# Performance work log

Hardware: AMD Instinct MI355X
Metric: run time of the kernel (lower is better)

The kernel has to match this reference:

```python
import jax, jax.numpy as jnp
import numpy as np

N = 20000      # nodes
E = 320000     # edges (avg degree 16)
IN = 512       # input feature dim
HID = 64       # hidden_dim
NH = 8         # n_heads
NC = 20        # n_classes
NG = 64        # graphs in batch
EPS = 1e-5     # batchnorm eps


def setup_inputs() -> dict:
    key = jax.random.key(0)
    ks = jax.random.split(key, 32)
    rn = lambda k, shape, s=0.05: (jax.random.normal(k, shape, jnp.float32) * s)
    inp = {
        "x": rn(ks[0], (N, IN), 1.0),
        "src": jax.random.randint(ks[1], (E,), 0, N),
        "dst": jax.random.randint(ks[2], (E,), 0, N),
        "graph_ids": jnp.sort(jax.random.randint(ks[3], (N,), 0, NG)),
        "n_graphs": NG,
        # encoder
        "W_enc": rn(ks[4], (IN, HID)), "b_enc": jnp.zeros((HID,), jnp.float32),
        # GAT layer 0
        "fc_W0": rn(ks[5], (HID, NH * HID)),
        "attn_l0": rn(ks[6], (NH, HID)), "attn_r0": rn(ks[7], (NH, HID)),
        "res_W0": rn(ks[8], (HID, NH * HID)),
        "bias0": jnp.zeros((NH * HID,), jnp.float32),
        "dp_W0": rn(ks[9], (NH * HID, HID)), "dp_b0": jnp.zeros((HID,), jnp.float32),
        # GAT layer 1
        "fc_W1": rn(ks[10], (HID, NH * HID)),
        "attn_l1": rn(ks[11], (NH, HID)), "attn_r1": rn(ks[12], (NH, HID)),
        "res_W1": rn(ks[13], (HID, NH * HID)),
        "bias1": jnp.zeros((NH * HID,), jnp.float32),
        "dp_W1": rn(ks[14], (NH * HID, HID)), "dp_b1": jnp.zeros((HID,), jnp.float32),
        # batchnorm affine
        "gamma": jnp.ones((2 * HID,), jnp.float32), "beta": jnp.zeros((2 * HID,), jnp.float32),
        # global attention pooling gate
        "gate_W": rn(ks[15], (2 * HID, 1)), "gate_b": jnp.zeros((1,), jnp.float32),
        # classifier
        "cls_W": rn(ks[16], (2 * HID, NC)), "cls_b": jnp.zeros((NC,), jnp.float32),
    }
    return inp


def gat_conv(h, fc_W, attn_l, attn_r, res_W, bias, src, dst, n_nodes):
    # DGL GATConv: fc -> per-head scalar scores -> edge softmax over incoming
    # edges -> weighted sum -> residual + bias -> leaky_relu activation.
    nh, d = attn_l.shape
    feat = (h @ fc_W).reshape(n_nodes, nh, d)              # [N,H,D]
    el = jnp.sum(feat * attn_l[None], axis=-1)             # [N,H]
    er = jnp.sum(feat * attn_r[None], axis=-1)             # [N,H]
    e = jax.nn.leaky_relu(el[src] + er[dst], 0.2)          # [E,H]
    m = jax.ops.segment_max(e, dst, num_segments=n_nodes)  # segment softmax
    ex = jnp.exp(e - m[dst])
    denom = jax.ops.segment_sum(ex, dst, num_segments=n_nodes)
    a = ex / denom[dst]                                    # [E,H]
    msg = feat[src] * a[:, :, None]                        # [E,H,D]  (dominant)
    rst = jax.ops.segment_sum(msg, dst, num_segments=n_nodes)  # [N,H,D]
    rst = rst + (h @ res_W).reshape(n_nodes, nh, d) + bias.reshape(nh, d)
    return jax.nn.leaky_relu(rst, 0.01)  # F.leaky_relu default slope


def reference(x, W_enc, b_enc,
              fc_W0, attn_l0, attn_r0, res_W0, bias0, dp_W0, dp_b0,
              fc_W1, attn_l1, attn_r1, res_W1, bias1, dp_W1, dp_b1,
              gamma, beta, gate_W, gate_b, cls_W, cls_b,
              src, dst, graph_ids, n_graphs):
    n_nodes = x.shape[0]
    he = x @ W_enc + b_enc                                  # encoder [N,HID]
    h = he
    h = gat_conv(h, fc_W0, attn_l0, attn_r0, res_W0, bias0, src, dst, n_nodes)
    h = h.reshape(n_nodes, -1) @ dp_W0 + dp_b0              # down_proj 0
    h = gat_conv(h, fc_W1, attn_l1, attn_r1, res_W1, bias1, src, dst, n_nodes)
    h = h.reshape(n_nodes, -1) @ dp_W1 + dp_b1              # down_proj 1
    hg = jnp.concatenate([h, he], axis=1)                   # [N,2*HID]
    # BatchNorm1d (training-mode batch stats, biased variance)
    mu = jnp.mean(hg, axis=0)
    var = jnp.var(hg, axis=0)
    hg = (hg - mu) * jax.lax.rsqrt(var + EPS) * gamma + beta
    # GlobalAttentionPooling: per-graph softmax over node gates
    gate = hg @ gate_W + gate_b                             # [N,1]
    gm = jax.ops.segment_max(gate, graph_ids, num_segments=n_graphs)
    ge = jnp.exp(gate - gm[graph_ids])
    gden = jax.ops.segment_sum(ge, graph_ids, num_segments=n_graphs)
    alpha = ge / gden[graph_ids]                            # [N,1]
    readout = jax.ops.segment_sum(alpha * hg, graph_ids, num_segments=n_graphs)
    return readout @ cls_W + cls_b                          # [NG,NC]
```

## Files before the change

### kernel.cpp

```cpp
#include <hip/hip_runtime.h>
#include <hip/hip_bf16.h>

#define MROWS   20000
#define N_EDGES 320000
#define DIN     512
#define HID     64
#define NH      8
#define ND      512
#define NCLS    20
#define NG      64
#define BN_EPS  1e-5f
#define PCH     16
#define BNB     256

typedef __hip_bfloat16 bf16;
typedef __attribute__((ext_vector_type(8))) short s16x8;
typedef __attribute__((ext_vector_type(4))) float f32x4;

enum { TF32 = 0, TBF16 = 1, TMODE = 2 };

__device__ __forceinline__ int getmode(const void* gamma) {
    return *(const unsigned*)gamma != 0x3F800000u;
}

__device__ __forceinline__ float ld_f32(const void* p, size_t i) { return ((const float*)p)[i]; }
__device__ __forceinline__ float ld_b16(const void* p, size_t i) { return __bfloat162float(((const bf16*)p)[i]); }

template<int T>
__device__ __forceinline__ float ldT(const void* p, size_t i, int bf) {
    if constexpr (T == TF32) return ld_f32(p, i);
    else if constexpr (T == TBF16) return ld_b16(p, i);
    else return bf ? ld_b16(p, i) : ld_f32(p, i);
}
template<int T>
__device__ __forceinline__ void stT(void* p, size_t i, int bf, float v) {
    if constexpr (T == TF32) ((float*)p)[i] = v;
    else if constexpr (T == TBF16) ((bf16*)p)[i] = __float2bfloat16(v);
    else { if (bf) ((bf16*)p)[i] = __float2bfloat16(v); else ((float*)p)[i] = v; }
}

__device__ __forceinline__ float bfbits2f(short s) {
    return __uint_as_float(((unsigned)(unsigned short)s) << 16);
}
__device__ __forceinline__ short f2bfbits(float v) {
    bf16 b = __float2bfloat16(v);
    return *reinterpret_cast<short*>(&b);
}

struct TP { const void* src[7]; bf16* dst[7]; int K[7]; };
__global__ void transpose7_kernel(TP tp, const void* __restrict__ gamma) {
    const int bf = getmode(gamma);
    int id = blockIdx.y;
    int i = blockIdx.x * 256 + threadIdx.x;
    int K = tp.K[id];
    int N = (DIN * HID) / K;
    int n = i / K, k = i - n * K;
    tp.dst[id][i] = __float2bfloat16(ldT<TMODE>(tp.src[id], (size_t)k * N + n, bf));
}

__global__ void convx_kernel(const void* __restrict__ x, bf16* __restrict__ xb,
                             const void* __restrict__ gamma) {
    if (getmode(gamma)) return;
    const int total4 = MROWS * DIN / 4;
    for (int i4 = blockIdx.x * 256 + threadIdx.x; i4 < total4; i4 += gridDim.x * 256) {
        float4 v = ((const float4*)x)[i4];
        int i = i4 * 4;
        xb[i + 0] = __float2bfloat16(v.x);
        xb[i + 1] = __float2bfloat16(v.y);
        xb[i + 2] = __float2bfloat16(v.z);
        xb[i + 3] = __float2bfloat16(v.w);
    }
}

__global__ void hist_kernel(const int* __restrict__ keys, int* __restrict__ counts, int n) {
    int i = blockIdx.x * 256 + threadIdx.x;
    if (i < n) atomicAdd(&counts[keys[i]], 1);
}

__global__ void gsearch_kernel(const int* __restrict__ gids, int* __restrict__ goffs) {
    int g = threadIdx.x;
    if (g > NG) return;
    int lo = 0, hi = MROWS;
    while (lo < hi) {
        int mid = (lo + hi) >> 1;
        if (gids[mid] < g) lo = mid + 1; else hi = mid;
    }
    goffs[g] = lo;
}

__global__ __launch_bounds__(1024)
void scan_kernel(const int* __restrict__ in, int* __restrict__ out) {
    const int C = 20;
    int t = threadIdx.x;
    int beg = t * C; if (beg > MROWS) beg = MROWS;
    int end = beg + C; if (end > MROWS) end = MROWS;
    int s = 0;
    for (int i = beg; i < end; ++i) s += in[i];
    int lane = t & 63, wid = t >> 6;
    int ps = s;
    #pragma unroll
    for (int o = 1; o < 64; o <<= 1) { int u = __shfl_up(ps, o, 64); if (lane >= o) ps += u; }
    __shared__ int wsum[16];
    if (lane == 63) wsum[wid] = ps;
    __syncthreads();
    if (wid == 0 && lane < 16) {
        int u = wsum[lane];
        #pragma unroll
        for (int o = 1; o < 16; o <<= 1) { int v = __shfl_up(u, o, 64); if (lane >= o) u += v; }
        wsum[lane] = u;
    }
    __syncthreads();
    int carry = ps - s + (wid > 0 ? wsum[wid - 1] : 0);
    int run = carry;
    for (int i = beg; i < end; ++i) { out[i] = run; run += in[i]; }
    if (t == 0) out[MROWS] = N_EDGES;
}

__global__ void scatter_kernel(const int* __restrict__ src, const int* __restrict__ dst,
                               const int* __restrict__ offs, int* __restrict__ cursor,
                               int* __restrict__ src_sorted) {
    int e = blockIdx.x * 256 + threadIdx.x;
    if (e < N_EDGES) {
        int d = dst[e];
        int pos = offs[d] + atomicAdd(&cursor[d], 1);
        src_sorted[pos] = src[e];
    }
}

template<int K, int NB, int NTOT>
__global__ __launch_bounds__(256)
void gemm_mfma(const void* __restrict__ Araw, const bf16* __restrict__ Aconv,
               const bf16* __restrict__ BT, const void* __restrict__ bias,
               bf16* __restrict__ C, const void* __restrict__ gamma) {
    const int bf = getmode(gamma);
    const bf16* A = bf ? (const bf16*)Araw : Aconv;
    const int wid  = threadIdx.x >> 6;
    const int lane = threadIdx.x & 63;
    const int quad = lane >> 4;
    const int l16  = lane & 15;
    const int rb = blockIdx.x * 128 + wid * 32;
    const int cb = blockIdx.y * NB;
    constexpr int CT = NB / 16;
    constexpr int KC = K / 32;

    f32x4 acc[2][CT] = {};
    int r0 = rb + l16;       if (r0 >= MROWS) r0 = MROWS - 1;
    int r1 = rb + 16 + l16;  if (r1 >= MROWS) r1 = MROWS - 1;
    const bf16* a0p = A + (size_t)r0 * K + quad * 8;
    const bf16* a1p = A + (size_t)r1 * K + quad * 8;
    const bf16* btp = BT + (size_t)(cb + l16) * K + quad * 8;

    for (int kc = 0; kc < KC; ++kc) {
        s16x8 af0 = *(const s16x8*)(a0p + kc * 32);
        s16x8 af1 = *(const s16x8*)(a1p + kc * 32);
        s16x8 bfr[CT];
        #pragma unroll
        for (int ct = 0; ct < CT; ++ct)
            bfr[ct] = *(const s16x8*)(btp + (size_t)ct * 16 * K + kc * 32);
        #pragma unroll
        for (int ct = 0; ct < CT; ++ct) {
            acc[0][ct] = __builtin_amdgcn_mfma_f32_16x16x32_bf16(af0, bfr[ct], acc[0][ct], 0, 0, 0);
            acc[1][ct] = __builtin_amdgcn_mfma_f32_16x16x32_bf16(af1, bfr[ct], acc[1][ct], 0, 0, 0);
        }
    }
    #pragma unroll
    for (int ct = 0; ct < CT; ++ct) {
        int col = cb + ct * 16 + l16;
        float bb = bias ? ldT<TMODE>(bias, col, bf) : 0.f;
        #pragma unroll
        for (int rt = 0; rt < 2; ++rt) {
            #pragma unroll
            for (int rg = 0; rg < 4; ++rg) {
                int row = rb + rt * 16 + quad * 4 + rg;
                if (row < MROWS)
                    C[(size_t)row * NTOT + col] = __float2bfloat16(acc[rt][ct][rg] + bb);
            }
        }
    }
}

__global__ __launch_bounds__(256)
void gemm_fcres(const bf16* __restrict__ A, const bf16* __restrict__ BT_fc,
                const bf16* __restrict__ BT_res, const void* __restrict__ bias,
                const void* __restrict__ attn_l, const void* __restrict__ attn_r,
                bf16* __restrict__ feat, bf16* __restrict__ rst,
                float* __restrict__ el, float* __restrict__ er,
                const void* __restrict__ gamma) {
    const int bf = getmode(gamma);
    const bool isres = blockIdx.y >= 4;
    const int yy = blockIdx.y & 3;
    const bf16* BT = isres ? BT_res : BT_fc;
    bf16* C = isres ? rst : feat;
    const int wid  = threadIdx.x >> 6;
    const int lane = threadIdx.x & 63;
    const int quad = lane >> 4;
    const int l16  = lane & 15;
    const int rb = blockIdx.x * 128 + wid * 32;
    const int cb = yy * 128;
    constexpr int CT = 8;
    constexpr int K  = HID;
    constexpr int KC = K / 32;

    f32x4 acc[2][CT] = {};
    int r0 = rb + l16;       if (r0 >= MROWS) r0 = MROWS - 1;
    int r1 = rb + 16 + l16;  if (r1 >= MROWS) r1 = MROWS - 1;
    const bf16* a0p = A + (size_t)r0 * K + quad * 8;
    const bf16* a1p = A + (size_t)r1 * K + quad * 8;
    const bf16* btp = BT + (size_t)(cb + l16) * K + quad * 8;

    #pragma unroll
    for (int kc = 0; kc < KC; ++kc) {
        s16x8 af0 = *(const s16x8*)(a0p + kc * 32);
        s16x8 af1 = *(const s16x8*)(a1p + kc * 32);
        s16x8 bfr[CT];
        #pragma unroll
        for (int ct = 0; ct < CT; ++ct)
            bfr[ct] = *(const s16x8*)(btp + (size_t)ct * 16 * K + kc * 32);
        #pragma unroll
        for (int ct = 0; ct < CT; ++ct) {
            acc[0][ct] = __builtin_amdgcn_mfma_f32_16x16x32_bf16(af0, bfr[ct], acc[0][ct], 0, 0, 0);
            acc[1][ct] = __builtin_amdgcn_mfma_f32_16x16x32_bf16(af1, bfr[ct], acc[1][ct], 0, 0, 0);
        }
    }
    #pragma unroll
    for (int ct = 0; ct < CT; ++ct) {
        int col = cb + ct * 16 + l16;
        float bb = isres ? ldT<TMODE>(bias, col, bf) : 0.f;
        #pragma unroll
        for (int rt = 0; rt < 2; ++rt) {
            #pragma unroll
            for (int rg = 0; rg < 4; ++rg) {
                int row = rb + rt * 16 + quad * 4 + rg;
                if (row < MROWS)
                    C[(size_t)row * ND + col] = __float2bfloat16(acc[rt][ct][rg] + bb);
            }
        }
    }
    if (!isres) {
        float al[CT], ar[CT];
        #pragma unroll
        for (int ct = 0; ct < CT; ++ct) {
            int col = cb + ct * 16 + l16;
            al[ct] = ldT<TMODE>(attn_l, col, bf);
            ar[ct] = ldT<TMODE>(attn_r, col, bf);
        }
        #pragma unroll
        for (int rt = 0; rt < 2; ++rt) {
            #pragma unroll
            for (int rg = 0; rg < 4; ++rg) {
                float e0 = 0.f, e1 = 0.f, f0 = 0.f, f1 = 0.f;
                #pragma unroll
                for (int ct = 0; ct < 4; ++ct) {
                    e0 += acc[rt][ct][rg] * al[ct];
                    f0 += acc[rt][ct][rg] * ar[ct];
                    e1 += acc[rt][ct + 4][rg] * al[ct + 4];
                    f1 += acc[rt][ct + 4][rg] * ar[ct + 4];
                }
                #pragma unroll
                for (int o = 1; o < 16; o <<= 1) {
                    e0 += __shfl_xor(e0, o, 64);
                    e1 += __shfl_xor(e1, o, 64);
                    f0 += __shfl_xor(f0, o, 64);
                    f1 += __shfl_xor(f1, o, 64);
                }
                int row = rb + rt * 16 + quad * 4 + rg;
                if (row < MROWS) {
                    if (l16 == 0) { el[row * 8 + 2 * yy] = e0;     er[row * 8 + 2 * yy] = f0; }
                    if (l16 == 1) { el[row * 8 + 2 * yy + 1] = e1; er[row * 8 + 2 * yy + 1] = f1; }
                }
            }
        }
    }
}

__global__ __launch_bounds__(256)
void agg_kernel(const bf16* __restrict__ feat, const float* __restrict__ el,
                const float* __restrict__ er, const int* __restrict__ offs,
                const int* __restrict__ srcs, bf16* __restrict__ rst) {
    int gid = blockIdx.x * 256 + threadIdx.x;
    int n = gid >> 6;
    int l = threadIdx.x & 63;
    if (n >= MROWS) return;
    int hh = l >> 3;
    int hw = l & 7;
    int e0 = offs[n], e1 = offs[n + 1];
    float er_w = er[n * 8 + hw];
    float acc[8] = {0.f, 0.f, 0.f, 0.f, 0.f, 0.f, 0.f, 0.f};
    float den = 0.f;
    const bf16* fcol = feat + l * 8;

    for (int base = e0; base < e1; base += 8) {
        int m = e1 - base; if (m > 8) m = 8;
        int sv = (base + hw < e1) ? srcs[base + hw] : 0;
        int sj = __shfl(sv, l >> 3, 64);
        float sc = el[sj * 8 + hw] + er_w;
        sc = sc > 0.f ? sc : 0.2f * sc;
        float w = ((l >> 3) < m) ? __expf(fminf(sc, 30.f)) : 0.f;
        if (m == 8) {
            s16x8 rows[8];
            float ws[8];
            #pragma unroll
            for (int j = 0; j < 8; ++j) {
                int s = __shfl(sv, j, 64);
                rows[j] = *(const s16x8*)(fcol + (size_t)s * ND);
                ws[j] = __shfl(w, (j << 3) | hh, 64);
            }
            #pragma unroll
            for (int j = 0; j < 8; ++j) {
                den += ws[j];
                #pragma unroll
                for (int k = 0; k < 8; ++k)
                    acc[k] += bfbits2f(rows[j][k]) * ws[j];
            }
        } else {
            for (int j = 0; j < m; ++j) {
                int s = __shfl(sv, j, 64);
                float wj = __shfl(w, (j << 3) | hh, 64);
                s16x8 f8 = *(const s16x8*)(fcol + (size_t)s * ND);
                den += wj;
                #pragma unroll
                for (int k = 0; k < 8; ++k)
                    acc[k] += bfbits2f(f8[k]) * wj;
            }
        }
    }
    float inv = (den > 0.f) ? 1.f / den : 0.f;
    s16x8* rp = (s16x8*)(rst + (size_t)n * ND + l * 8);
    s16x8 rr = *rp;
    s16x8 ro;
    #pragma unroll
    for (int j = 0; j < 8; ++j) {
        float r = bfbits2f(rr[j]) + acc[j] * inv;
        r = r > 0.f ? r : 0.01f * r;
        ro[j] = f2bfbits(r);
    }
    *rp = ro;
}

__global__ void bn_part_kernel(const bf16* __restrict__ h2, const bf16* __restrict__ he,
                               float* __restrict__ psum, float* __restrict__ psq) {
    int t = threadIdx.x;
    int b = blockIdx.x;
    int beg = (int)((long)MROWS * b / BNB);
    int end = (int)((long)MROWS * (b + 1) / BNB);
    const bf16* srcb = (t < 64) ? h2 : he;
    int col = t & 63;
    float s = 0.f, s2 = 0.f;
    for (int r = beg; r < end; ++r) {
        float v = __bfloat162float(srcb[(size_t)r * 64 + col]);
        s += v;
        s2 += v * v;
    }
    psum[b * 128 + t] = s;
    psq[b * 128 + t] = s2;
}

__global__ void bn_reduce_kernel(const float* __restrict__ psum, const float* __restrict__ psq,
                                 const void* __restrict__ gamma, const void* __restrict__ beta,
                                 float* __restrict__ scale, float* __restrict__ shift) {
    const int bf = getmode(gamma);
    int t = threadIdx.x;
    float s = 0.f, s2 = 0.f;
    for (int b = 0; b < BNB; ++b) { s += psum[b * 128 + t]; s2 += psq[b * 128 + t]; }
    float mu = s * (1.f / MROWS);
    float var = s2 * (1.f / MROWS) - mu * mu;
    float inv = rsqrtf(fmaxf(var, 0.f) + BN_EPS);
    float a = ldT<TMODE>(gamma, t, bf) * inv;
    scale[t] = a;
    shift[t] = ldT<TMODE>(beta, t, bf) - mu * a;
}

__global__ __launch_bounds__(256)
void gate_kernel(const bf16* __restrict__ h2, const bf16* __restrict__ he,
                 const float* __restrict__ scale, const float* __restrict__ shift,
                 const void* __restrict__ gate_W, const void* __restrict__ gate_b,
                 float* __restrict__ ge, const void* __restrict__ gamma) {
    const int bf = getmode(gamma);
    int gid = blockIdx.x * 256 + threadIdx.x;
    int r = gid >> 6;
    int l = threadIdx.x & 63;
    if (r >= MROWS) return;
    float v0 = __bfloat162float(h2[(size_t)r * 64 + l]) * scale[l] + shift[l];
    float v1 = __bfloat162float(he[(size_t)r * 64 + l]) * scale[64 + l] + shift[64 + l];
    float s = v0 * ldT<TMODE>(gate_W, l, bf) + v1 * ldT<TMODE>(gate_W, 64 + l, bf);
    #pragma unroll
    for (int o = 32; o > 0; o >>= 1) s += __shfl_xor(s, o, 64);
    if (l == 0) {
        float g = s + ldT<TMODE>(gate_b, 0, bf);
        ge[r] = __expf(fminf(fmaxf(g, -60.f), 30.f));
    }
}

__global__ void pool1_kernel(const bf16* __restrict__ h2, const bf16* __restrict__ he,
                             const float* __restrict__ scale, const float* __restrict__ shift,
                             const float* __restrict__ ge, const int* __restrict__ goffs,
                             float* __restrict__ pacc, float* __restrict__ pden) {
    int g = blockIdx.x;
    int c = blockIdx.y;
    int t = threadIdx.x;
    int r0 = goffs[g], r1 = goffs[g + 1];
    int len = r1 - r0;
    int beg = r0 + (int)((long)len * c / PCH);
    int end = r0 + (int)((long)len * (c + 1) / PCH);
    const bf16* srcb = (t < 64) ? h2 : he;
    int col = t & 63;
    float sc = scale[t], sh = shift[t];
    float acc = 0.f, den = 0.f;
    for (int r = beg; r < end; ++r) {
        float wg = ge[r];
        float v = __bfloat162float(srcb[(size_t)r * 64 + col]) * sc + sh;
        den += wg;
        acc += wg * v;
    }
    pacc[((size_t)g * PCH + c) * 128 + t] = acc;
    if (t == 0) pden[g * PCH + c] = den;
}

__global__ void pool2cls_kernel(const float* __restrict__ pacc, const float* __restrict__ pden,
                                const void* __restrict__ W, const void* __restrict__ b,
                                void* __restrict__ out, const void* __restrict__ gamma) {
    const int bf = getmode(gamma);
    int g = blockIdx.x;
    int t = threadIdx.x;
    float acc = 0.f, den = 0.f;
    #pragma unroll
    for (int c = 0; c < PCH; ++c) {
        acc += pacc[((size_t)g * PCH + c) * 128 + t];
        den += pden[g * PCH + c];
    }
    __shared__ float ro[128];
    ro[t] = (den > 0.f) ? acc / den : 0.f;
    __syncthreads();
    if (t < NCLS) {
        float s = ldT<TMODE>(b, t, bf);
        #pragma unroll 8
        for (int k = 0; k < 128; ++k)
            s += ro[k] * ldT<TMODE>(W, k * NCLS + t, bf);
        stT<TMODE>(out, g * NCLS + t, bf, s);
    }
}

extern "C" void kernel_launch(void* const* d_in, const int* in_sizes, int n_in,
                              void* d_out, int out_size, void* d_ws, size_t ws_size,
                              hipStream_t stream) {
    const void* x       = d_in[0];
    const int*  src     = (const int*)d_in[1];
    const int*  dst     = (const int*)d_in[2];
    const int*  gids    = (const int*)d_in[3];
    const void* W_enc   = d_in[5];
    const void* b_enc   = d_in[6];
    const void* fc_W0   = d_in[7];
    const void* attn_l0 = d_in[8];
    const void* attn_r0 = d_in[9];
    const void* res_W0  = d_in[10];
    const void* bias0   = d_in[11];
    const void* dp_W0   = d_in[12];
    const void* dp_b0   = d_in[13];
    const void* fc_W1   = d_in[14];
    const void* attn_l1 = d_in[15];
    const void* attn_r1 = d_in[16];
    const void* res_W1  = d_in[17];
    const void* bias1   = d_in[18];
    const void* dp_W1   = d_in[19];
    const void* dp_b1   = d_in[20];
    const void* gamma   = d_in[21];
    const void* beta    = d_in[22];
    const void* gate_W  = d_in[23];
    const void* gate_b  = d_in[24];
    const void* cls_W   = d_in[25];
    const void* cls_b   = d_in[26];

    char* wsc = (char*)d_ws;
    size_t off = 0;
    auto alloc = [&](size_t bytes) -> void* {
        void* p = wsc + off;
        off = (off + bytes + 255) & ~(size_t)255;
        return p;
    };
    bf16*  he        = (bf16*) alloc((size_t)MROWS * HID * 2);
    bf16*  h         = (bf16*) alloc((size_t)MROWS * HID * 2);
    bf16*  h2        = (bf16*) alloc((size_t)MROWS * HID * 2);
    bf16*  feat      = (bf16*) alloc((size_t)MROWS * ND * 2);
    bf16*  rst       = (bf16*) alloc((size_t)MROWS * ND * 2);
    bf16*  xb        = rst;
    bf16*  bt_enc    = (bf16*) alloc((size_t)DIN * HID * 2);
    bf16*  bt_fc0    = (bf16*) alloc((size_t)HID * ND * 2);
    bf16*  bt_res0   = (bf16*) alloc((size_t)HID * ND * 2);
    bf16*  bt_dp0    = (bf16*) alloc((size_t)ND * HID * 2);
    bf16*  bt_fc1    = (bf16*) alloc((size_t)HID * ND * 2);
    bf16*  bt_res1   = (bf16*) alloc((size_t)HID * ND * 2);
    bf16*  bt_dp1    = (bf16*) alloc((size_t)ND * HID * 2);
    float* el        = (float*)alloc((size_t)MROWS * 8 * 4);
    float* er        = (float*)alloc((size_t)MROWS * 8 * 4);
    float* ge        = (float*)alloc((size_t)MROWS * 4);
    int*   src_sorted= (int*)  alloc((size_t)N_EDGES * 4);
    int*   offs      = (int*)  alloc((size_t)(MROWS + 1) * 4);
    int*   goffs     = (int*)  alloc((size_t)(NG + 1) * 4);
    float* psum      = (float*)alloc((size_t)BNB * 128 * 4);
    float* psq       = (float*)alloc((size_t)BNB * 128 * 4);
    float* pacc      = (float*)alloc((size_t)NG * PCH * 128 * 4);
    float* pden      = (float*)alloc((size_t)NG * PCH * 4);
    float* bnscale   = (float*)alloc(128 * 4);
    float* bnshift   = (float*)alloc(128 * 4);
    size_t zbytes = (size_t)MROWS * 4 * 2;
    char*  zbase  = (char*)alloc(zbytes);
    int* counts  = (int*)zbase;
    int* cursor  = counts + MROWS;

    hipMemsetAsync(zbase, 0, zbytes, stream);

    TP tp;
    tp.src[0] = W_enc;  tp.K[0] = DIN;
    tp.src[1] = fc_W0;  tp.K[1] = HID;
    tp.src[2] = res_W0; tp.K[2] = HID;
    tp.src[3] = dp_W0;  tp.K[3] = ND;
    tp.src[4] = fc_W1;  tp.K[4] = HID;
    tp.src[5] = res_W1; tp.K[5] = HID;
    tp.src[6] = dp_W1;  tp.K[6] = ND;
    tp.dst[0] = bt_enc; tp.dst[1] = bt_fc0; tp.dst[2] = bt_res0; tp.dst[3] = bt_dp0;
    tp.dst[4] = bt_fc1; tp.dst[5] = bt_res1; tp.dst[6] = bt_dp1;
    transpose7_kernel<<<dim3((DIN * HID) / 256, 7), 256, 0, stream>>>(tp, gamma);
    convx_kernel<<<640, 256, 0, stream>>>(x, xb, gamma);

    hist_kernel<<<(N_EDGES + 255) / 256, 256, 0, stream>>>(dst, counts, N_EDGES);
    gsearch_kernel<<<1, 128, 0, stream>>>(gids, goffs);
    scan_kernel<<<1, 1024, 0, stream>>>(counts, offs);
    scatter_kernel<<<(N_EDGES + 255) / 256, 256, 0, stream>>>(src, dst, offs, cursor, src_sorted);

    const int GX = (MROWS + 127) / 128;

    gemm_mfma<DIN, 64, 64><<<dim3(GX, 1), 256, 0, stream>>>(x, xb, bt_enc, b_enc, he, gamma);

    gemm_fcres<<<dim3(GX, 8), 256, 0, stream>>>(he, bt_fc0, bt_res0, bias0, attn_l0, attn_r0,
                                                feat, rst, el, er, gamma);
    agg_kernel<<<(MROWS * 64) / 256, 256, 0, stream>>>(feat, el, er, offs, src_sorted, rst);
    gemm_mfma<ND, 64, 64><<<dim3(GX, 1), 256, 0, stream>>>(rst, rst, bt_dp0, dp_b0, h, gamma);

    gemm_fcres<<<dim3(GX, 8), 256, 0, stream>>>(h, bt_fc1, bt_res1, bias1, attn_l1, attn_r1,
                                                feat, rst, el, er, gamma);
    agg_kernel<<<(MROWS * 64) / 256, 256, 0, stream>>>(feat, el, er, offs, src_sorted, rst);
    gemm_mfma<ND, 64, 64><<<dim3(GX, 1), 256, 0, stream>>>(rst, rst, bt_dp1, dp_b1, h2, gamma);

    bn_part_kernel<<<BNB, 128, 0, stream>>>(h2, he, psum, psq);
    bn_reduce_kernel<<<1, 128, 0, stream>>>(psum, psq, gamma, beta, bnscale, bnshift);
    gate_kernel<<<(MROWS * 64 + 255) / 256, 256, 0, stream>>>(h2, he, bnscale, bnshift, gate_W, gate_b, ge, gamma);
    pool1_kernel<<<dim3(NG, PCH), 128, 0, stream>>>(h2, he, bnscale, bnshift, ge, goffs, pacc, pden);
    pool2cls_kernel<<<NG, 128, 0, stream>>>(pacc, pden, cls_W, cls_b, d_out, gamma);
}
```

Baseline: 487.5 us.

## Split-K the skinny GEMMs and restructure edge aggregation per head slice

The N=64 projection GEMMs (encoder and down-projections) now split K into four slices over a second grid dimension, write fp32 partials into a scratch buffer that aliases feat, and sum them with bias in a separate add-convert kernel. The aggregation kernel now assigns each block one head slice of 16 nodes, with lanes processing 8 edges in parallel, and reduces across lanes with shuffles. Both changes aim to raise parallelism and occupancy on the wide GPU. The cost is extra fp32 partial traffic plus an additional launch per GEMM, and aggregation re-reads edge indices and el once per head.

```diff
diff --git a/kernel.cpp b/kernel.cpp
--- a/kernel.cpp
+++ b/kernel.cpp
@@ -12,6 +12,7 @@
 #define BN_EPS  1e-5f
 #define PCH     16
 #define BNB     256
+#define KS      4
 
 typedef __hip_bfloat16 bf16;
 typedef __attribute__((ext_vector_type(8))) short s16x8;
@@ -127,56 +128,56 @@
     }
 }
 
-template<int K, int NB, int NTOT>
+template<int K>
 __global__ __launch_bounds__(256)
-void gemm_mfma(const void* __restrict__ Araw, const bf16* __restrict__ Aconv,
-               const bf16* __restrict__ BT, const void* __restrict__ bias,
-               bf16* __restrict__ C, const void* __restrict__ gamma) {
+void gemm_nk(const void* __restrict__ Araw, const bf16* __restrict__ Aconv,
+             const bf16* __restrict__ BT, float* __restrict__ Ctmp,
+             const void* __restrict__ gamma) {
     const int bf = getmode(gamma);
     const bf16* A = bf ? (const bf16*)Araw : Aconv;
     const int wid  = threadIdx.x >> 6;
     const int lane = threadIdx.x & 63;
     const int quad = lane >> 4;
     const int l16  = lane & 15;
-    const int rb = blockIdx.x * 128 + wid * 32;
-    const int cb = blockIdx.y * NB;
-    constexpr int CT = NB / 16;
-    constexpr int KC = K / 32;
-
-    f32x4 acc[2][CT] = {};
-    int r0 = rb + l16;       if (r0 >= MROWS) r0 = MROWS - 1;
-    int r1 = rb + 16 + l16;  if (r1 >= MROWS) r1 = MROWS - 1;
-    const bf16* a0p = A + (size_t)r0 * K + quad * 8;
-    const bf16* a1p = A + (size_t)r1 * K + quad * 8;
-    const bf16* btp = BT + (size_t)(cb + l16) * K + quad * 8;
-
+    const int rb = blockIdx.x * 64 + wid * 16;
+    const int kz = blockIdx.y * (K / KS);
+    constexpr int KC = (K / KS) / 32;
+
+    f32x4 acc[4] = {};
+    int r0 = rb + l16; if (r0 >= MROWS) r0 = MROWS - 1;
+    const bf16* ap = A + (size_t)r0 * K + kz + quad * 8;
+    const bf16* btp = BT + (size_t)l16 * K + kz + quad * 8;
+
+    #pragma unroll
     for (int kc = 0; kc < KC; ++kc) {
-        s16x8 af0 = *(const s16x8*)(a0p + kc * 32);
-        s16x8 af1 = *(const s16x8*)(a1p + kc * 32);
-        s16x8 bfr[CT];
-        #pragma unroll
-        for (int ct = 0; ct < CT; ++ct)
-            bfr[ct] = *(const s16x8*)(btp + (size_t)ct * 16 * K + kc * 32);
-        #pragma unroll
-        for (int ct = 0; ct < CT; ++ct) {
-            acc[0][ct] = __builtin_amdgcn_mfma_f32_16x16x32_bf16(af0, bfr[ct], acc[0][ct], 0, 0, 0);
-            acc[1][ct] = __builtin_amdgcn_mfma_f32_16x16x32_bf16(af1, bfr[ct], acc[1][ct], 0, 0, 0);
-        }
-    }
-    #pragma unroll
-    for (int ct = 0; ct < CT; ++ct) {
-        int col = cb + ct * 16 + l16;
-        float bb = bias ? ldT<TMODE>(bias, col, bf) : 0.f;
-        #pragma unroll
-        for (int rt = 0; rt < 2; ++rt) {
-            #pragma unroll
-            for (int rg = 0; rg < 4; ++rg) {
-                int row = rb + rt * 16 + quad * 4 + rg;
-                if (row < MROWS)
-                    C[(size_t)row * NTOT + col] = __float2bfloat16(acc[rt][ct][rg] + bb);
-            }
-        }
-    }
+        s16x8 af = *(const s16x8*)(ap + kc * 32);
+        #pragma unroll
+        for (int ct = 0; ct < 4; ++ct) {
+            s16x8 bfr = *(const s16x8*)(btp + (size_t)ct * 16 * K + kc * 32);
+            acc[ct] = __builtin_amdgcn_mfma_f32_16x16x32_bf16(af, bfr, acc[ct], 0, 0, 0);
+        }
+    }
+    float* cz = Ctmp + (size_t)blockIdx.y * MROWS * 64;
+    #pragma unroll
+    for (int ct = 0; ct < 4; ++ct) {
+        int col = ct * 16 + l16;
+        #pragma unroll
+        for (int rg = 0; rg < 4; ++rg) {
+            int row = rb + quad * 4 + rg;
+            if (row < MROWS) cz[(size_t)row * 64 + col] = acc[ct][rg];
+        }
+    }
+}
+
+__global__ void addcvt_kernel(const float* __restrict__ Ctmp, const void* __restrict__ bias,
+                              bf16* __restrict__ out, const void* __restrict__ gamma) {
+    const int bf = getmode(gamma);
+    int i = blockIdx.x * 256 + threadIdx.x;
+    if (i >= MROWS * 64) return;
+    float v = ldT<TMODE>(bias, i & 63, bf);
+    #pragma unroll
+    for (int z = 0; z < KS; ++z) v += Ctmp[(size_t)z * MROWS * 64 + i];
+    out[i] = __float2bfloat16(v);
 }
 
 __global__ __launch_bounds__(256)
@@ -277,64 +278,56 @@
 void agg_kernel(const bf16* __restrict__ feat, const float* __restrict__ el,
                 const float* __restrict__ er, const int* __restrict__ offs,
                 const int* __restrict__ srcs, bf16* __restrict__ rst) {
-    int gid = blockIdx.x * 256 + threadIdx.x;
-    int n = gid >> 6;
-    int l = threadIdx.x & 63;
-    if (n >= MROWS) return;
-    int hh = l >> 3;
-    int hw = l & 7;
-    int e0 = offs[n], e1 = offs[n + 1];
-    float er_w = er[n * 8 + hw];
-    float acc[8] = {0.f, 0.f, 0.f, 0.f, 0.f, 0.f, 0.f, 0.f};
-    float den = 0.f;
-    const bf16* fcol = feat + l * 8;
-
-    for (int base = e0; base < e1; base += 8) {
-        int m = e1 - base; if (m > 8) m = 8;
-        int sv = (base + hw < e1) ? srcs[base + hw] : 0;
-        int sj = __shfl(sv, l >> 3, 64);
-        float sc = el[sj * 8 + hw] + er_w;
-        sc = sc > 0.f ? sc : 0.2f * sc;
-        float w = ((l >> 3) < m) ? __expf(fminf(sc, 30.f)) : 0.f;
-        if (m == 8) {
-            s16x8 rows[8];
-            float ws[8];
+    const int s = blockIdx.x & 7;
+    const int chunk = blockIdx.x >> 3;
+    const int wid = threadIdx.x >> 6;
+    const int l = threadIdx.x & 63;
+    const int j = l >> 3;
+    const int c = l & 7;
+    const bf16* fslice = feat + s * 64 + c * 8;
+
+    int nbase = chunk * 16 + wid * 4;
+    #pragma unroll
+    for (int ni = 0; ni < 4; ++ni) {
+        int n = nbase + ni;
+        if (n >= MROWS) return;
+        int e0 = offs[n], e1 = offs[n + 1];
+        float er_s = er[n * 8 + s];
+        float acc[8] = {0.f, 0.f, 0.f, 0.f, 0.f, 0.f, 0.f, 0.f};
+        float den = 0.f;
+        for (int base = e0; base < e1; base += 8) {
+            int idx = base + j;
+            bool valid = idx < e1;
+            int sj = valid ? srcs[idx] : 0;
+            float sc = el[sj * 8 + s] + er_s;
+            sc = sc > 0.f ? sc : 0.2f * sc;
+            float w = valid ? __expf(fminf(sc, 30.f)) : 0.f;
+            s16x8 f8 = *(const s16x8*)(fslice + (size_t)sj * ND);
+            den += w;
             #pragma unroll
-            for (int j = 0; j < 8; ++j) {
-                int s = __shfl(sv, j, 64);
-                rows[j] = *(const s16x8*)(fcol + (size_t)s * ND);
-                ws[j] = __shfl(w, (j << 3) | hh, 64);
+            for (int k = 0; k < 8; ++k)
+                acc[k] += bfbits2f(f8[k]) * w;
+        }
+        #pragma unroll
+        for (int o = 8; o < 64; o <<= 1) {
+            den += __shfl_xor(den, o, 64);
+            #pragma unroll
+            for (int k = 0; k < 8; ++k) acc[k] += __shfl_xor(acc[k], o, 64);
+        }
+        if (j == 0) {
+            float inv = (den > 0.f) ? 1.f / den : 0.f;
+            s16x8* rp = (s16x8*)(rst + (size_t)n * ND + s * 64 + c * 8);
+            s16x8 rr = *rp;
+            s16x8 ro;
+            #pragma unroll
+            for (int k = 0; k < 8; ++k) {
+                float r = bfbits2f(rr[k]) + acc[k] * inv;
+                r = r > 0.f ? r : 0.01f * r;
+                ro[k] = f2bfbits(r);
             }
-            #pragma unroll
-            for (int j = 0; j < 8; ++j) {
-                den += ws[j];
-                #pragma unroll
-                for (int k = 0; k < 8; ++k)
-                    acc[k] += bfbits2f(rows[j][k]) * ws[j];
-            }
-        } else {
-            for (int j = 0; j < m; ++j) {
-                int s = __shfl(sv, j, 64);
-                float wj = __shfl(w, (j << 3) | hh, 64);
-                s16x8 f8 = *(const s16x8*)(fcol + (size_t)s * ND);
-                den += wj;
-                #pragma unroll
-                for (int k = 0; k < 8; ++k)
-                    acc[k] += bfbits2f(f8[k]) * wj;
-            }
-        }
-    }
-    float inv = (den > 0.f) ? 1.f / den : 0.f;
-    s16x8* rp = (s16x8*)(rst + (size_t)n * ND + l * 8);
-    s16x8 rr = *rp;
-    s16x8 ro;
-    #pragma unroll
-    for (int j = 0; j < 8; ++j) {
-        float r = bfbits2f(rr[j]) + acc[j] * inv;
-        r = r > 0.f ? r : 0.01f * r;
-        ro[j] = f2bfbits(r);
-    }
-    *rp = ro;
+            *rp = ro;
+        }
+    }
 }
 
 __global__ void bn_part_kernel(const bf16* __restrict__ h2, const bf16* __restrict__ he,
@@ -483,6 +476,7 @@
     bf16*  feat      = (bf16*) alloc((size_t)MROWS * ND * 2);
     bf16*  rst       = (bf16*) alloc((size_t)MROWS * ND * 2);
     bf16*  xb        = rst;
+    float* Ctmp      = (float*)feat;
     bf16*  bt_enc    = (bf16*) alloc((size_t)DIN * HID * 2);
     bf16*  bt_fc0    = (bf16*) alloc((size_t)HID * ND * 2);
     bf16*  bt_res0   = (bf16*) alloc((size_t)HID * ND * 2);
@@ -527,19 +521,25 @@
     scan_kernel<<<1, 1024, 0, stream>>>(counts, offs);
     scatter_kernel<<<(N_EDGES + 255) / 256, 256, 0, stream>>>(src, dst, offs, cursor, src_sorted);
 
-    const int GX = (MROWS + 127) / 128;
-
-    gemm_mfma<DIN, 64, 64><<<dim3(GX, 1), 256, 0, stream>>>(x, xb, bt_enc, b_enc, he, gamma);
+    const int GX  = (MROWS + 127) / 128;
+    const int GXN = (MROWS + 63) / 64;
+    const int GAGG = ((MROWS + 15) / 16) * 8;
+    const int GADD = (MROWS * 64 + 255) / 256;
+
+    gemm_nk<DIN><<<dim3(GXN, KS), 256, 0, stream>>>(x, xb, bt_enc, Ctmp, gamma);
+    addcvt_kernel<<<GADD, 256, 0, stream>>>(Ctmp, b_enc, he, gamma);
 
     gemm_fcres<<<dim3(GX, 8), 256, 0, stream>>>(he, bt_fc0, bt_res0, bias0, attn_l0, attn_r0,
                                                 feat, rst, el, er, gamma);
-    agg_kernel<<<(MROWS * 64) / 256, 256, 0, stream>>>(feat, el, er, offs, src_sorted, rst);
-    gemm_mfma<ND, 64, 64><<<dim3(GX, 1), 256, 0, stream>>>(rst, rst, bt_dp0, dp_b0, h, gamma);
+    agg_kernel<<<GAGG, 256, 0, stream>>>(feat, el, er, offs, src_sorted, rst);
+    gemm_nk<ND><<<dim3(GXN, KS), 256, 0, stream>>>(rst, rst, bt_dp0, Ctmp, gamma);
+    addcvt_kernel<<<GADD, 256, 0, stream>>>(Ctmp, dp_b0, h, gamma);
 
     gemm_fcres<<<dim3(GX, 8), 256, 0, stream>>>(h, bt_fc1, bt_res1, bias1, attn_l1, attn_r1,
                                                 feat, rst, el, er, gamma);
-    agg_kernel<<<(MROWS * 64) / 256, 256, 0, stream>>>(feat, el, er, offs, src_sorted, rst);
-    gemm_mfma<ND, 64, 64><<<dim3(GX, 1), 256, 0, stream>>>(rst, rst, bt_dp1, dp_b1, h2, gamma);
+    agg_kernel<<<GAGG, 256, 0, stream>>>(feat, el, er, offs, src_sorted, rst);
+    gemm_nk<ND><<<dim3(GXN, KS), 256, 0, stream>>>(rst, rst, bt_dp1, Ctmp, gamma);
+    addcvt_kernel<<<GADD, 256, 0, stream>>>(Ctmp, dp_b1, h2, gamma);
 
     bn_part_kernel<<<BNB, 128, 0, stream>>>(h2, he, psum, psq);
     bn_reduce_kernel<<<1, 128, 0, stream>>>(psum, psq, gamma, beta, bnscale, bnshift);
```

New measurement: 550.9 us. 13.0% more time.

## Split edge-softmax weight computation from aggregation and slice aggregation per head

Applied to the files above, without the earlier changes.

Edge attention weights and per-node reciprocal denominators are now computed in a separate kernel and stored head-major in a new global buffer. The aggregation kernel is reorganised so each block handles one head's 64-column slice for 16 nodes, with lanes spread over 8 edges by 8 column groups. Partial sums are reduced with shuffles before the residual and activation writeback. This is meant to make feature gathers land in one head slice per block for better cache locality and to remove the per-edge shuffles, at the cost of an extra launch and an extra write and read of the weight array.

```diff
diff --git a/kernel.cpp b/kernel.cpp
--- a/kernel.cpp
+++ b/kernel.cpp
@@ -274,67 +274,81 @@
 }
 
 __global__ __launch_bounds__(256)
-void agg_kernel(const bf16* __restrict__ feat, const float* __restrict__ el,
-                const float* __restrict__ er, const int* __restrict__ offs,
-                const int* __restrict__ srcs, bf16* __restrict__ rst) {
+void wcomp_kernel(const float* __restrict__ el, const float* __restrict__ er,
+                  const int* __restrict__ offs, const int* __restrict__ srcs,
+                  float* __restrict__ wT, float* __restrict__ deninv) {
     int gid = blockIdx.x * 256 + threadIdx.x;
     int n = gid >> 6;
     int l = threadIdx.x & 63;
     if (n >= MROWS) return;
-    int hh = l >> 3;
-    int hw = l & 7;
+    int j = l >> 3, hw = l & 7;
     int e0 = offs[n], e1 = offs[n + 1];
-    float er_w = er[n * 8 + hw];
-    float acc[8] = {0.f, 0.f, 0.f, 0.f, 0.f, 0.f, 0.f, 0.f};
-    float den = 0.f;
-    const bf16* fcol = feat + l * 8;
-
+    float er_h = er[n * 8 + hw];
+    float dsum = 0.f;
     for (int base = e0; base < e1; base += 8) {
-        int m = e1 - base; if (m > 8) m = 8;
-        int sv = (base + hw < e1) ? srcs[base + hw] : 0;
-        int sj = __shfl(sv, l >> 3, 64);
-        float sc = el[sj * 8 + hw] + er_w;
+        int idx = base + j;
+        bool valid = idx < e1;
+        int sj = valid ? srcs[idx] : 0;
+        float sc = el[sj * 8 + hw] + er_h;
         sc = sc > 0.f ? sc : 0.2f * sc;
-        float w = ((l >> 3) < m) ? __expf(fminf(sc, 30.f)) : 0.f;
-        if (m == 8) {
-            s16x8 rows[8];
-            float ws[8];
+        float w = valid ? __expf(fminf(sc, 30.f)) : 0.f;
+        if (valid) wT[(size_t)hw * N_EDGES + idx] = w;
+        dsum += w;
+    }
+    #pragma unroll
+    for (int o = 8; o < 64; o <<= 1) dsum += __shfl_xor(dsum, o, 64);
+    if (j == 0) deninv[n * 8 + hw] = (dsum > 0.f) ? 1.f / dsum : 0.f;
+}
+
+__global__ __launch_bounds__(256)
+void agg_kernel(const bf16* __restrict__ feat, const float* __restrict__ wT,
+                const float* __restrict__ deninv, const int* __restrict__ offs,
+                const int* __restrict__ srcs, bf16* __restrict__ rst) {
+    const int s = blockIdx.x & 7;
+    const int chunk = blockIdx.x >> 3;
+    const int wid = threadIdx.x >> 6;
+    const int l = threadIdx.x & 63;
+    const int j = l >> 3;
+    const int c = l & 7;
+    const bf16* fslice = feat + s * 64 + c * 8;
+    const float* wS = wT + (size_t)s * N_EDGES;
+
+    int nbase = chunk * 16 + wid * 4;
+    #pragma unroll
+    for (int ni = 0; ni < 4; ++ni) {
+        int n = nbase + ni;
+        if (n >= MROWS) return;
+        int e0 = offs[n], e1 = offs[n + 1];
+        float acc[8] = {0.f, 0.f, 0.f, 0.f, 0.f, 0.f, 0.f, 0.f};
+        for (int base = e0; base < e1; base += 8) {
+            int idx = base + j;
+            bool valid = idx < e1;
+            int sj = valid ? srcs[idx] : 0;
+            float w = valid ? wS[idx] : 0.f;
+            s16x8 f8 = *(const s16x8*)(fslice + (size_t)sj * ND);
             #pragma unroll
-            for (int j = 0; j < 8; ++j) {
-                int s = __shfl(sv, j, 64);
-                rows[j] = *(const s16x8*)(fcol + (size_t)s * ND);
-                ws[j] = __shfl(w, (j << 3) | hh, 64);
+            for (int k = 0; k < 8; ++k)
+                acc[k] += bfbits2f(f8[k]) * w;
+        }
+        #pragma unroll
+        for (int o = 8; o < 64; o <<= 1) {
+            #pragma unroll
+            for (int k = 0; k < 8; ++k) acc[k] += __shfl_xor(acc[k], o, 64);
+        }
+        if (j == 0) {
+            float inv = deninv[n * 8 + s];
+            s16x8* rp = (s16x8*)(rst + (size_t)n * ND + s * 64 + c * 8);
+            s16x8 rr = *rp;
+            s16x8 ro;
+            #pragma unroll
+            for (int k = 0; k < 8; ++k) {
+                float r = bfbits2f(rr[k]) + acc[k] * inv;
+                r = r > 0.f ? r : 0.01f * r;
+                ro[k] = f2bfbits(r);
             }
-            #pragma unroll
-            for (int j = 0; j < 8; ++j) {
-                den += ws[j];
-                #pragma unroll
-                for (int k = 0; k < 8; ++k)
-                    acc[k] += bfbits2f(rows[j][k]) * ws[j];
-            }
-        } else {
-            for (int j = 0; j < m; ++j) {
-                int s = __shfl(sv, j, 64);
-                float wj = __shfl(w, (j << 3) | hh, 64);
-                s16x8 f8 = *(const s16x8*)(fcol + (size_t)s * ND);
-                den += wj;
-                #pragma unroll
-                for (int k = 0; k < 8; ++k)
-                    acc[k] += bfbits2f(f8[k]) * wj;
-            }
-        }
-    }
-    float inv = (den > 0.f) ? 1.f / den : 0.f;
-    s16x8* rp = (s16x8*)(rst + (size_t)n * ND + l * 8);
-    s16x8 rr = *rp;
-    s16x8 ro;
-    #pragma unroll
-    for (int j = 0; j < 8; ++j) {
-        float r = bfbits2f(rr[j]) + acc[j] * inv;
-        r = r > 0.f ? r : 0.01f * r;
-        ro[j] = f2bfbits(r);
-    }
-    *rp = ro;
+            *rp = ro;
+        }
+    }
 }
 
 __global__ void bn_part_kernel(const bf16* __restrict__ h2, const bf16* __restrict__ he,
@@ -492,6 +506,8 @@
     bf16*  bt_dp1    = (bf16*) alloc((size_t)ND * HID * 2);
     float* el        = (float*)alloc((size_t)MROWS * 8 * 4);
     float* er        = (float*)alloc((size_t)MROWS * 8 * 4);
+    float* wT        = (float*)alloc((size_t)NH * N_EDGES * 4);
+    float* deninv    = (float*)alloc((size_t)MROWS * 8 * 4);
     float* ge        = (float*)alloc((size_t)MROWS * 4);
     int*   src_sorted= (int*)  alloc((size_t)N_EDGES * 4);
     int*   offs      = (int*)  alloc((size_t)(MROWS + 1) * 4);
@@ -528,17 +544,21 @@
     scatter_kernel<<<(N_EDGES + 255) / 256, 256, 0, stream>>>(src, dst, offs, cursor, src_sorted);
 
     const int GX = (MROWS + 127) / 128;
+    const int GW = (MROWS * 64) / 256;
+    const int GAGG = ((MROWS + 15) / 16) * 8;
 
     gemm_mfma<DIN, 64, 64><<<dim3(GX, 1), 256, 0, stream>>>(x, xb, bt_enc, b_enc, he, gamma);
 
     gemm_fcres<<<dim3(GX, 8), 256, 0, stream>>>(he, bt_fc0, bt_res0, bias0, attn_l0, attn_r0,
                                                 feat, rst, el, er, gamma);
-    agg_kernel<<<(MROWS * 64) / 256, 256, 0, stream>>>(feat, el, er, offs, src_sorted, rst);
+    wcomp_kernel<<<GW, 256, 0, stream>>>(el, er, offs, src_sorted, wT, deninv);
+    agg_kernel<<<GAGG, 256, 0, stream>>>(feat, wT, deninv, offs, src_sorted, rst);
     gemm_mfma<ND, 64, 64><<<dim3(GX, 1), 256, 0, stream>>>(rst, rst, bt_dp0, dp_b0, h, gamma);
 
     gemm_fcres<<<dim3(GX, 8), 256, 0, stream>>>(h, bt_fc1, bt_res1, bias1, attn_l1, attn_r1,
                                                 feat, rst, el, er, gamma);
-    agg_kernel<<<(MROWS * 64) / 256, 256, 0, stream>>>(feat, el, er, offs, src_sorted, rst);
+    wcomp_kernel<<<GW, 256, 0, stream>>>(el, er, offs, src_sorted, wT, deninv);
+    agg_kernel<<<GAGG, 256, 0, stream>>>(feat, wT, deninv, offs, src_sorted, rst);
     gemm_mfma<ND, 64, 64><<<dim3(GX, 1), 256, 0, stream>>>(rst, rst, bt_dp1, dp_b1, h2, gamma);
 
     bn_part_kernel<<<BNB, 128, 0, stream>>>(h2, he, psum, psq);
```

Result: slower. 532.7 us (+9.3%).
